# Kernel optimization log

Hardware: AMD Instinct MI355X
Metric: run time of the kernel (lower is better)

The kernel has to match this reference:

```python
import jax, jax.numpy as jnp
import numpy as np

D_MODEL = 2048

def setup_inputs() -> dict:
    key = jax.random.key(0)
    kx, kw, kb = jax.random.split(key, 3)
    B, T, D = 4, 4096, D_MODEL
    x = jax.random.normal(kx, (B, T, D), dtype=jnp.float32)
    # torch nn.Linear(D, 3D): weight (3D, D), bias (3D); store transposed for x @ W
    scale = 1.0 / np.sqrt(D)
    W = jax.random.uniform(kw, (D, 3 * D), dtype=jnp.float32, minval=-scale, maxval=scale)
    b = jax.random.uniform(kb, (3 * D,), dtype=jnp.float32, minval=-scale, maxval=scale)
    return {"x": x, "W": W, "b": b}

def reference(x, W, b):
    # x: (B, T, D)
    qkv = x @ W + b                      # (B, T, 3D)
    q, k, v = jnp.split(qkv, 3, axis=-1) # each (B, T, D)
    # Original rearranges to (b, d, n, 1) then norms over dim=-2 == sequence axis n
    qn = q / jnp.linalg.norm(q, axis=1, keepdims=True)  # L2 norm over T
    kn = k / jnp.linalg.norm(k, axis=1, keepdims=True)
    kv = jnp.sum(kn * v, axis=1, keepdims=True)         # (B, 1, D) per-channel scalar
    return qn * kv                                      # (B, T, D)
```

## Files before the change

kernel.cpp:

```cpp
#include <hip/hip_runtime.h>
#include <hip/hip_bf16.h>
#include <stdint.h>


#define DMODEL 2048
#define TSEQ   4096
#define MM     16384
#define NN     6144
#define KK     2048

typedef unsigned short u16;
typedef __bf16 bf16x8 __attribute__((ext_vector_type(8)));
typedef float  f32x4  __attribute__((ext_vector_type(4)));
typedef u16    u16x8  __attribute__((ext_vector_type(8)));

__device__ __forceinline__ u16 f2bf(float f) {
    unsigned u = __float_as_uint(f);
    u += 0x7fffu + ((u >> 16) & 1u);
    return (u16)(u >> 16);
}
__device__ __forceinline__ float bf2f(u16 h) {
    return __uint_as_float(((unsigned)h) << 16);
}

__global__ void cvt_x_kernel(const float* __restrict__ x, u16* __restrict__ xb) {
    long i = ((long)blockIdx.x * 256 + threadIdx.x) * 8;
    float4 a = *(const float4*)(x + i);
    float4 b = *(const float4*)(x + i + 4);
    u16x8 o;
    o[0] = f2bf(a.x); o[1] = f2bf(a.y); o[2] = f2bf(a.z); o[3] = f2bf(a.w);
    o[4] = f2bf(b.x); o[5] = f2bf(b.y); o[6] = f2bf(b.z); o[7] = f2bf(b.w);
    *(u16x8*)(xb + i) = o;
}

__global__ void cvt_wt_kernel(const float* __restrict__ W, u16* __restrict__ wt) {
    __shared__ u16 tile[64][65];
    const int k0 = blockIdx.x * 64;
    const int n0 = blockIdx.y * 64;
    const int t  = threadIdx.x;
#pragma unroll
    for (int p = 0; p < 16; ++p) {
        int idx = p * 256 + t;
        int kk = idx >> 6, nn = idx & 63;
        tile[kk][nn] = f2bf(W[(long)(k0 + kk) * NN + n0 + nn]);
    }
    __syncthreads();
#pragma unroll
    for (int p = 0; p < 16; ++p) {
        int idx = p * 256 + t;
        int nn = idx >> 6, kk = idx & 63;
        wt[(long)(n0 + nn) * KK + k0 + kk] = tile[kk][nn];
    }
}

#define BAR()   __builtin_amdgcn_s_barrier()
#define VMW(n)  asm volatile("s_waitcnt vmcnt(" #n ")" ::: "memory")
#define PRIO(x) __builtin_amdgcn_s_setprio(x)

__global__ __launch_bounds__(512, 2) void gemm_qkv_pl(
        const u16* __restrict__ xb, const u16* __restrict__ wt,
        const float* __restrict__ bias, u16* __restrict__ qb,
        u16* __restrict__ kb, u16* __restrict__ vb, float* __restrict__ sums) {
    __shared__ u16 smem[2][2][256 * 64];

    const int tid = threadIdx.x;
    const int l = tid & 63, w = tid >> 6;
    const int wm = w >> 2, wn = w & 3;
    const int lr = l & 15, lk = l >> 4;

    int bid = (int)blockIdx.x;
    int swz = (bid & 7) * (1536 / 8) + (bid >> 3);
    const int m0 = (swz & 63) * 256;
    const int n0 = (swz >> 6) * 256;

    const int srow = w * 8 + (l >> 3);
    const int sc8  = l & 7;

    const int cxor = lr & 7;
    const int aoff0 = (wm * 128 + lr) * 64 + ((0 + lk) ^ cxor) * 8;
    const int aoff1 = (wm * 128 + lr) * 64 + ((4 + lk) ^ cxor) * 8;
    const int boff0 = (wn * 64 + lr) * 64 + ((0 + lk) ^ cxor) * 8;
    const int boff1 = (wn * 64 + lr) * 64 + ((4 + lk) ^ cxor) * 8;

    const int cl = sc8 ^ (srow & 7);
    const u16* gA0 = xb + (long)(m0 +   0 + srow) * KK + cl * 8;
    const u16* gA1 = xb + (long)(m0 +  64 + srow) * KK + cl * 8;
    const u16* gA2 = xb + (long)(m0 + 128 + srow) * KK + cl * 8;
    const u16* gA3 = xb + (long)(m0 + 192 + srow) * KK + cl * 8;
    const u16* gB0 = wt + (long)(n0 +   0 + srow) * KK + cl * 8;
    const u16* gB1 = wt + (long)(n0 +  64 + srow) * KK + cl * 8;
    const u16* gB2 = wt + (long)(n0 + 128 + srow) * KK + cl * 8;
    const u16* gB3 = wt + (long)(n0 + 192 + srow) * KK + cl * 8;

    f32x4 acc[8][4] = {};

#define STG_(buf, mat, qq, gp) __builtin_amdgcn_global_load_lds(               \
    (__attribute__((address_space(1))) void*)(u16*)(gp),                       \
    (__attribute__((address_space(3))) void*)&smem[buf][mat][(qq)*4096 + w*512], 16, 0, 0)

#define STAGE_ALL(buf) do {                                                    \
    STG_(buf, 1, 0, gB0); STG_(buf, 1, 1, gB1);                                \
    STG_(buf, 1, 2, gB2); STG_(buf, 1, 3, gB3);                                \
    STG_(buf, 0, 0, gA0); STG_(buf, 0, 1, gA1);                                \
    STG_(buf, 0, 2, gA2); STG_(buf, 0, 3, gA3);                                \
    gA0 += 64; gA1 += 64; gA2 += 64; gA3 += 64;                                \
    gB0 += 64; gB1 += 64; gB2 += 64; gB3 += 64; } while (0)

#define RDA(dst, Ab, p) do {                                                   \
    dst[0][0] = *(const bf16x8*)(Ab + aoff0 + ((p) * 32 +  0) * 64);           \
    dst[0][1] = *(const bf16x8*)(Ab + aoff1 + ((p) * 32 +  0) * 64);           \
    dst[1][0] = *(const bf16x8*)(Ab + aoff0 + ((p) * 32 + 16) * 64);           \
    dst[1][1] = *(const bf16x8*)(Ab + aoff1 + ((p) * 32 + 16) * 64); } while (0)

#define MFMAQ(p, Af)                                                           \
    PRIO(1);                                                                   \
    _Pragma("unroll")                                                          \
    for (int i_ = 0; i_ < 2; ++i_) {                                           \
        _Pragma("unroll")                                                      \
        for (int n_ = 0; n_ < 4; ++n_) {                                       \
            acc[(p)*2+i_][n_] = __builtin_amdgcn_mfma_f32_16x16x32_bf16(       \
                Af[i_][0], Bf[n_][0], acc[(p)*2+i_][n_], 0, 0, 0);             \
            acc[(p)*2+i_][n_] = __builtin_amdgcn_mfma_f32_16x16x32_bf16(       \
                Af[i_][1], Bf[n_][1], acc[(p)*2+i_][n_], 0, 0, 0);             \
        } }                                                                    \
    PRIO(0);

#define TILE(cb, nb, en_stage) do {                                            \
    if (en_stage) STAGE_ALL(nb);                                               \
    const u16* Ab = &smem[cb][0][0];                                           \
    const u16* Bb = &smem[cb][1][0];                                           \
    bf16x8 Bf[4][2], Af0[2][2], Af1[2][2];                                     \
    _Pragma("unroll")                                                          \
    for (int n_ = 0; n_ < 4; ++n_) {                                           \
        Bf[n_][0] = *(const bf16x8*)(Bb + boff0 + n_ * 1024);                  \
        Bf[n_][1] = *(const bf16x8*)(Bb + boff1 + n_ * 1024);                  \
    }                                                                          \
    RDA(Af0, Ab, 0); RDA(Af1, Ab, 1);                                          \
    MFMAQ(0, Af0)                                                              \
    RDA(Af0, Ab, 2);                                                           \
    MFMAQ(1, Af1)                                                              \
    RDA(Af1, Ab, 3);                                                           \
    MFMAQ(2, Af0)                                                              \
    MFMAQ(3, Af1)                                                              \
    VMW(0); BAR(); } while (0)

    STAGE_ALL(0);
    VMW(0); BAR();

    for (int t = 0; t < 32; t += 2) {
        TILE(0, 1, true);
        TILE(1, 0, (t + 2 < 32));
    }

    float bv[4];
#pragma unroll
    for (int n_ = 0; n_ < 4; ++n_) bv[n_] = bias[n0 + wn * 64 + n_ * 16 + lr];

    const bool isq = (n0 < DMODEL);
    const bool isk = (n0 >= DMODEL) && (n0 < 2 * DMODEL);
    float psum[4] = {0.f, 0.f, 0.f, 0.f};

#pragma unroll
    for (int mi = 0; mi < 8; ++mi) {
#pragma unroll
        for (int n_ = 0; n_ < 4; ++n_) {
            int gn = n0 + wn * 64 + n_ * 16 + lr;
#pragma unroll
            for (int j = 0; j < 4; ++j) {
                int gm = m0 + wm * 128 + mi * 16 + lk * 4 + j;
                float val = acc[mi][n_][j] + bv[n_];
                if (isq) {
                    qb[(long)gm * DMODEL + gn] = f2bf(val);
                    psum[n_] += val * val;
                } else if (isk) {
                    kb[(long)gm * DMODEL + (gn - DMODEL)] = f2bf(val);
                    psum[n_] += val * val;
                } else {
                    vb[(long)gm * DMODEL + (gn - 2 * DMODEL)] = f2bf(val);
                }
            }
        }
    }

    if (n0 < 2 * DMODEL) {
        const int roff = isq ? 0 : 8192;
        const int bb   = m0 >> 12;
        const int dbase = (n0 - (isq ? 0 : DMODEL)) + wn * 64;
#pragma unroll
        for (int n_ = 0; n_ < 4; ++n_) {
            float v = psum[n_];
            v += __shfl_xor(v, 32);
            v += __shfl_xor(v, 16);
            if (lk == 0)
                atomicAdd(&sums[roff + bb * DMODEL + dbase + n_ * 16 + lr], v);
        }
    }
#undef STG_
#undef STAGE_ALL
#undef RDA
#undef MFMAQ
#undef TILE
}

__global__ void kv_kernel(const u16* __restrict__ kb, const u16* __restrict__ vb,
                          float* __restrict__ sums) {
    const int b  = blockIdx.x >> 7;
    const int tc = blockIdx.x & 127;
    const long row0 = (long)b * TSEQ + tc * 32;
    const int d0 = threadIdx.x * 8;
    float akv[8] = {};
    for (int r = 0; r < 32; ++r) {
        long base = (row0 + r) * (long)DMODEL + d0;
        u16x8 k8 = *(const u16x8*)(kb + base);
        u16x8 v8 = *(const u16x8*)(vb + base);
#pragma unroll
        for (int j = 0; j < 8; ++j)
            akv[j] += bf2f(k8[j]) * bf2f(v8[j]);
    }
    const int sbase = b * DMODEL + d0;
#pragma unroll
    for (int j = 0; j < 8; ++j)
        atomicAdd(&sums[16384 + sbase + j], akv[j]);
}

__global__ void finalize_kernel(const float* __restrict__ sums, float* __restrict__ s) {
    int i = blockIdx.x * 256 + threadIdx.x;
    float sqq = sums[i], skk = sums[8192 + i], skv = sums[16384 + i];
    s[i] = skv / sqrtf(sqq * skk);
}

__global__ void scale_kernel(const u16* __restrict__ qb, float* __restrict__ out,
                             const float* __restrict__ s) {
    long e = ((long)blockIdx.x * 256 + threadIdx.x) * 8;
    int d = (int)(e & (DMODEL - 1));
    int b = (int)(e >> 23);
    u16x8 q8 = *(const u16x8*)(qb + e);
    float4 s0 = *(const float4*)(s + b * DMODEL + d);
    float4 s1 = *(const float4*)(s + b * DMODEL + d + 4);
    float4 o0, o1;
    o0.x = bf2f(q8[0]) * s0.x; o0.y = bf2f(q8[1]) * s0.y;
    o0.z = bf2f(q8[2]) * s0.z; o0.w = bf2f(q8[3]) * s0.w;
    o1.x = bf2f(q8[4]) * s1.x; o1.y = bf2f(q8[5]) * s1.y;
    o1.z = bf2f(q8[6]) * s1.z; o1.w = bf2f(q8[7]) * s1.w;
    *(float4*)(out + e) = o0;
    *(float4*)(out + e + 4) = o1;
}

extern "C" void kernel_launch(void* const* d_in, const int* in_sizes, int n_in,
                              void* d_out, int out_size, void* d_ws, size_t ws_size,
                              hipStream_t stream) {
    const float* x    = (const float*)d_in[0];
    const float* W    = (const float*)d_in[1];
    const float* bias = (const float*)d_in[2];
    float* out = (float*)d_out;

    char* ws = (char*)d_ws;
    u16*   xb   = (u16*)(ws);
    u16*   wt   = (u16*)(ws + 67108864L);
    u16*   kb   = (u16*)(ws + 92274688L);
    u16*   vb   = (u16*)(ws + 159383552L);
    u16*   qb   = (u16*)(ws + 226492416L);
    float* sums = (float*)(ws + 293601280L);
    float* sc   = (float*)(ws + 293601280L + 98304L);

    hipMemsetAsync(sums, 0, 3 * 8192 * sizeof(float), stream);
    cvt_x_kernel<<<16384, 256, 0, stream>>>(x, xb);
    cvt_wt_kernel<<<dim3(KK / 64, NN / 64), 256, 0, stream>>>(W, wt);
    gemm_qkv_pl<<<1536, 512, 0, stream>>>(xb, wt, bias, qb, kb, vb, sums);
    kv_kernel<<<512, 256, 0, stream>>>(kb, vb, sums);
    finalize_kernel<<<32, 256, 0, stream>>>(sums, sc);
    scale_kernel<<<16384, 256, 0, stream>>>(qb, out, sc);
}
```

Measured before the change: 533.6 us.

## Interleave partial A/B tile staging with MFMA phases in QKV GEMM

```diff
diff --git a/kernel.cpp b/kernel.cpp
--- a/kernel.cpp
+++ b/kernel.cpp
@@ -54,10 +54,12 @@
 }
 
 #define BAR()   __builtin_amdgcn_s_barrier()
+#define LGKM0() asm volatile("s_waitcnt lgkmcnt(0)" ::: "memory")
+#define LGKM8() asm volatile("s_waitcnt lgkmcnt(8)" ::: "memory")
 #define VMW(n)  asm volatile("s_waitcnt vmcnt(" #n ")" ::: "memory")
 #define PRIO(x) __builtin_amdgcn_s_setprio(x)
 
-__global__ __launch_bounds__(512, 2) void gemm_qkv_pl(
+__global__ __launch_bounds__(512, 2) void gemm_qkv_m2(
         const u16* __restrict__ xb, const u16* __restrict__ wt,
         const float* __restrict__ bias, u16* __restrict__ qb,
         u16* __restrict__ kb, u16* __restrict__ vb, float* __restrict__ sums) {
@@ -93,18 +95,16 @@
     const u16* gB3 = wt + (long)(n0 + 192 + srow) * KK + cl * 8;
 
     f32x4 acc[8][4] = {};
-
-#define STG_(buf, mat, qq, gp) __builtin_amdgcn_global_load_lds(               \
-    (__attribute__((address_space(1))) void*)(u16*)(gp),                       \
+    bf16x8 Bf[4][2];
+
+#define STG_(buf, mat, qq, gp, kofs) __builtin_amdgcn_global_load_lds(         \
+    (__attribute__((address_space(1))) void*)(u16*)((gp) + (kofs)),            \
     (__attribute__((address_space(3))) void*)&smem[buf][mat][(qq)*4096 + w*512], 16, 0, 0)
 
-#define STAGE_ALL(buf) do {                                                    \
-    STG_(buf, 1, 0, gB0); STG_(buf, 1, 1, gB1);                                \
-    STG_(buf, 1, 2, gB2); STG_(buf, 1, 3, gB3);                                \
-    STG_(buf, 0, 0, gA0); STG_(buf, 0, 1, gA1);                                \
-    STG_(buf, 0, 2, gA2); STG_(buf, 0, 3, gA3);                                \
-    gA0 += 64; gA1 += 64; gA2 += 64; gA3 += 64;                                \
-    gB0 += 64; gB1 += 64; gB2 += 64; gB3 += 64; } while (0)
+#define ST_A0(buf, kofs) do { STG_(buf,0,0,gA0,kofs); STG_(buf,0,1,gA1,kofs); } while (0)
+#define ST_A1(buf, kofs) do { STG_(buf,0,2,gA2,kofs); STG_(buf,0,3,gA3,kofs); } while (0)
+#define ST_B0(buf, kofs) do { STG_(buf,1,0,gB0,kofs); STG_(buf,1,1,gB1,kofs); } while (0)
+#define ST_B1(buf, kofs) do { STG_(buf,1,2,gB2,kofs); STG_(buf,1,3,gB3,kofs); } while (0)
 
 #define RDA(dst, Ab, p) do {                                                   \
     dst[0][0] = *(const bf16x8*)(Ab + aoff0 + ((p) * 32 +  0) * 64);           \
@@ -125,32 +125,46 @@
         } }                                                                    \
     PRIO(0);
 
-#define TILE(cb, nb, en_stage) do {                                            \
-    if (en_stage) STAGE_ALL(nb);                                               \
+#define TILE(cb, nb, enA, enB, WAITS) do {                                     \
     const u16* Ab = &smem[cb][0][0];                                           \
     const u16* Bb = &smem[cb][1][0];                                           \
-    bf16x8 Bf[4][2], Af0[2][2], Af1[2][2];                                     \
+    bf16x8 Af[2][2];                                                           \
+                         \
     _Pragma("unroll")                                                          \
     for (int n_ = 0; n_ < 4; ++n_) {                                           \
         Bf[n_][0] = *(const bf16x8*)(Bb + boff0 + n_ * 1024);                  \
         Bf[n_][1] = *(const bf16x8*)(Bb + boff1 + n_ * 1024);                  \
     }                                                                          \
-    RDA(Af0, Ab, 0); RDA(Af1, Ab, 1);                                          \
-    MFMAQ(0, Af0)                                                              \
-    RDA(Af0, Ab, 2);                                                           \
-    MFMAQ(1, Af1)                                                              \
-    RDA(Af1, Ab, 3);                                                           \
-    MFMAQ(2, Af0)                                                              \
-    MFMAQ(3, Af1)                                                              \
-    VMW(0); BAR(); } while (0)
-
-    STAGE_ALL(0);
-    VMW(0); BAR();
-
-    for (int t = 0; t < 32; t += 2) {
-        TILE(0, 1, true);
-        TILE(1, 0, (t + 2 < 32));
-    }
+    RDA(Af, Ab, 0);                                                            \
+    if (enA) ST_A0(nb, 64);                                                    \
+    LGKM8();                                                                   \
+    BAR(); LGKM0(); MFMAQ(0, Af) BAR();                                        \
+                                 \
+    RDA(Af, Ab, 1);                                                            \
+    if (enA) ST_A1(nb, 64);                                                    \
+    BAR(); LGKM0(); MFMAQ(1, Af) BAR();                                        \
+      \
+    RDA(Af, Ab, 2);                                                            \
+    if (enB) ST_B0(cb, 128);                                                   \
+    BAR(); LGKM0(); MFMAQ(2, Af) BAR();                                        \
+                  \
+    RDA(Af, Ab, 3);                                                            \
+    if (enB) ST_B1(cb, 128);                                                   \
+    BAR(); LGKM0(); MFMAQ(3, Af) WAITS; BAR();                                 \
+    gA0 += 64; gA1 += 64; gA2 += 64; gA3 += 64;                                \
+    gB0 += 64; gB1 += 64; gB2 += 64; gB3 += 64; } while (0)
+
+    ST_B0(0, 0); ST_B1(0, 0);
+    ST_A0(0, 0); ST_A1(0, 0);
+    ST_B0(1, 64); ST_B1(1, 64);
+    VMW(4); BAR();
+
+    for (int t = 0; t < 30; t += 2) {
+        TILE(0, 1, true, true, VMW(4));
+        TILE(1, 0, true, true, VMW(4));
+    }
+    TILE(0, 1, true, false, VMW(0));
+    TILE(1, 0, false, false, );
 
     float bv[4];
 #pragma unroll
@@ -196,7 +210,10 @@
         }
     }
 #undef STG_
-#undef STAGE_ALL
+#undef ST_A0
+#undef ST_A1
+#undef ST_B0
+#undef ST_B1
 #undef RDA
 #undef MFMAQ
 #undef TILE
@@ -266,7 +283,7 @@
     hipMemsetAsync(sums, 0, 3 * 8192 * sizeof(float), stream);
     cvt_x_kernel<<<16384, 256, 0, stream>>>(x, xb);
     cvt_wt_kernel<<<dim3(KK / 64, NN / 64), 256, 0, stream>>>(W, wt);
-    gemm_qkv_pl<<<1536, 512, 0, stream>>>(xb, wt, bias, qb, kb, vb, sums);
+    gemm_qkv_m2<<<1536, 512, 0, stream>>>(xb, wt, bias, qb, kb, vb, sums);
     kv_kernel<<<512, 256, 0, stream>>>(kb, vb, sums);
     finalize_kernel<<<32, 256, 0, stream>>>(sums, sc);
     scale_kernel<<<16384, 256, 0, stream>>>(qb, out, sc);
```

After: 540.1 us. Within noise of the previous version (+1.2%).
